# Kernel tuning notes

Hardware: AMD Instinct MI355X
Metric: run time of the kernel (lower is better)

The kernel has to match this reference:

```python
import jax, jax.numpy as jnp
import numpy as np

# Rain-rate balancing weights from the AccClearQPN repo; the loop uses the
# weight values themselves as the thresholds (faithful to compute_weights).
BALANCING_WEIGHTS = (1.0, 2.0, 5.0, 10.0, 30.0)
KSZ = 1  # kernel_size


def compute_weights(target, mask_f):
    w = jnp.full_like(target, BALANCING_WEIGHTS[0])
    for i in range(1, len(BALANCING_WEIGHTS)):
        w = w + (BALANCING_WEIGHTS[i] - BALANCING_WEIGHTS[i - 1]) * (
            target >= BALANCING_WEIGHTS[i]
        ).astype(target.dtype)
    return w * mask_f


def setup_inputs() -> dict:
    key = jax.random.key(0)
    k1, k2, k3 = jax.random.split(key, 3)
    S, B, H, W = 8, 16, 512, 512
    predicted = jax.random.uniform(k1, (S, B, H, W), dtype=jnp.float32) * 40.0
    target = jax.random.uniform(k2, (B, S, H, W), dtype=jnp.float32) * 40.0
    mask = jax.random.randint(k3, (B, S, H, W), 0, 2).astype(jnp.int32)
    return {"predicted": predicted, "target": target, "mask": mask}


def reference(predicted, target, mask):
    # predicted: [S,B,H,W]; target/mask: [B,S,H,W]
    S, B, H, W = predicted.shape
    pred = jnp.transpose(predicted, (1, 0, 2, 3))  # (B,S,H,W)
    weights = compute_weights(target, mask.astype(target.dtype))
    k = KSZ
    # zero-pad pred spatially; invalid shifted positions are masked to +inf below
    padded = jnp.pad(pred, ((0, 0), (0, 0), (k, k), (k, k)))
    ii = jnp.arange(H)
    jj = jnp.arange(W)
    # init = unshifted weighted abs diff (same as the (0,0) shift)
    loss2D = jnp.abs((target - pred) * weights)
    for x in range(-k, k + 1):
        vx = (ii + x >= 0) & (ii + x < H)
        for y in range(-k, k + 1):
            vy = (jj + y >= 0) & (jj + y < W)
            # pred sample at (i+x, j+y) for target pixel (i, j)
            pshift = padded[..., k + x : k + x + H, k + y : k + y + W]
            l = jnp.abs((target - pshift) * weights)
            l = jnp.where(vx[:, None] & vy[None, :], l, jnp.inf)
            loss2D = jnp.minimum(loss2D, l)
    return jnp.mean(loss2D)
```

## Files before the change

### kernel.cpp

```cpp
#include <hip/hip_runtime.h>

constexpr int S_DIM = 8;
constexpr int B_DIM = 16;
constexpr int H = 512;
constexpr int W = 512;
constexpr int PLANE = H * W;
constexpr long long NTOT = (long long)S_DIM * B_DIM * H * W;
constexpr int NGROUPS = (int)(NTOT / 4);
constexpr int GROUPS_PER_ROW = W / 4;
constexpr int GROUPS_PER_PLANE = PLANE / 4;

__device__ __forceinline__ float weight_of(float t) {
    float w = 1.0f;
    if (t >= 2.0f)  w = 2.0f;
    if (t >= 5.0f)  w = 5.0f;
    if (t >= 10.0f) w = 10.0f;
    if (t >= 30.0f) w = 30.0f;
    return w;
}

__device__ __forceinline__ float min3(float a, float b, float c) {
    return fminf(fminf(a, b), c);
}

__global__ __launch_bounds__(256)
void wmae_main(const float* __restrict__ pred,
               const float* __restrict__ targ,
               const int*   __restrict__ mask,
               double*      __restrict__ ws_sum) {
    const float BIG = 1e30f;
    float acc = 0.0f;

    const int stride = gridDim.x * blockDim.x;
    for (int gi = blockIdx.x * blockDim.x + threadIdx.x; gi < NGROUPS; gi += stride) {
        const int pl  = gi >> 16;
        const int rem = gi & (GROUPS_PER_PLANE - 1);
        const int row = rem >> 7;
        const int grp = rem & (GROUPS_PER_ROW - 1);
        const int j0  = grp << 2;

        const int b = pl >> 3;
        const int s = pl & 7;

        const size_t toff = (size_t)pl * PLANE + (size_t)row * W + j0;
        const float4 t4 = *reinterpret_cast<const float4*>(targ + toff);
        const int4   m4 = *reinterpret_cast<const int4*>(mask + toff);

        const float w0 = weight_of(t4.x) * (float)m4.x;
        const float w1 = weight_of(t4.y) * (float)m4.y;
        const float w2 = weight_of(t4.z) * (float)m4.z;
        const float w3 = weight_of(t4.w) * (float)m4.w;

        const float* pp = pred + (size_t)(s * B_DIM + b) * PLANE;

        float mn0 = BIG, mn1 = BIG, mn2 = BIG, mn3 = BIG;

        const int r_lo = (row > 0)     ? row - 1 : row;
        const int r_hi = (row < H - 1) ? row + 1 : row;

        for (int r = r_lo; r <= r_hi; ++r) {
            const float* pr = pp + (size_t)r * W + j0;
            const float4 p4 = *reinterpret_cast<const float4*>(pr);
            const float pv0 = (grp > 0)                  ? pr[-1] : BIG;
            const float pv5 = (grp < GROUPS_PER_ROW - 1) ? pr[4]  : BIG;
            const float pv1 = p4.x, pv2 = p4.y, pv3 = p4.z, pv4 = p4.w;

            mn0 = fminf(mn0, min3(fabsf(t4.x - pv0), fabsf(t4.x - pv1), fabsf(t4.x - pv2)));
            mn1 = fminf(mn1, min3(fabsf(t4.y - pv1), fabsf(t4.y - pv2), fabsf(t4.y - pv3)));
            mn2 = fminf(mn2, min3(fabsf(t4.z - pv2), fabsf(t4.z - pv3), fabsf(t4.z - pv4)));
            mn3 = fminf(mn3, min3(fabsf(t4.w - pv3), fabsf(t4.w - pv4), fabsf(t4.w - pv5)));
        }

        acc += w0 * mn0 + w1 * mn1 + w2 * mn2 + w3 * mn3;
    }

    #pragma unroll
    for (int off = 32; off > 0; off >>= 1)
        acc += __shfl_down(acc, off);

    __shared__ float wsum[4];
    const int wid  = threadIdx.x >> 6;
    const int lane = threadIdx.x & 63;
    if (lane == 0) wsum[wid] = acc;
    __syncthreads();
    if (threadIdx.x == 0) {
        const float bsum = wsum[0] + wsum[1] + wsum[2] + wsum[3];
        atomicAdd(ws_sum, (double)bsum);
    }
}

__global__ void wmae_finalize(const double* __restrict__ ws_sum,
                              float* __restrict__ out) {
    out[0] = (float)(ws_sum[0] / (double)NTOT);
}

extern "C" void kernel_launch(void* const* d_in, const int* in_sizes, int n_in,
                              void* d_out, int out_size, void* d_ws, size_t ws_size,
                              hipStream_t stream) {
    const float* predicted = (const float*)d_in[0];
    const float* target    = (const float*)d_in[1];
    const int*   mask      = (const int*)d_in[2];
    float* out  = (float*)d_out;
    double* wsd = (double*)d_ws;

    hipMemsetAsync(wsd, 0, sizeof(double), stream);
    wmae_main<<<2048, 256, 0, stream>>>(predicted, target, mask, wsd);
    wmae_finalize<<<1, 1, 0, stream>>>(wsd, out);
}
```

Measured before the change: 363.6 us.

## Assign wave per 4-row strip, reuse pred rows in registers, fuse finalize

Each wavefront now processes a 4-row strip of a plane, with each lane covering 8 columns. A rolling three-row register window keeps pred rows for reuse, and horizontal neighbours come from lane shuffles instead of extra unaligned loads. This cuts the redundant pred reads that the old per-group three-row loop made. The separate finalize kernel is replaced by a last-block-done counter inside the main kernel, which removes one launch but relies on correct fence and atomic ordering.

Measured after the change: 421.2 us. +15.8%, slower.

```diff
diff --git a/kernel.cpp b/kernel.cpp
--- a/kernel.cpp
+++ b/kernel.cpp
@@ -6,9 +6,14 @@
 constexpr int W = 512;
 constexpr int PLANE = H * W;
 constexpr long long NTOT = (long long)S_DIM * B_DIM * H * W;
-constexpr int NGROUPS = (int)(NTOT / 4);
-constexpr int GROUPS_PER_ROW = W / 4;
-constexpr int GROUPS_PER_PLANE = PLANE / 4;
+constexpr int ROWS = 4;
+constexpr int RBLKS = H / ROWS;
+constexpr int NPLANES = S_DIM * B_DIM;
+constexpr int NTASKS = NPLANES * RBLKS;
+constexpr int NBLOCKS = 2048;
+constexpr int NWAVES = NBLOCKS * 4;
+constexpr int TASKS_PER_WAVE = NTASKS / NWAVES;
+constexpr float BIG = 1e30f;
 
 __device__ __forceinline__ float weight_of(float t) {
     float w = 1.0f;
@@ -19,59 +24,109 @@
     return w;
 }
 
-__device__ __forceinline__ float min3(float a, float b, float c) {
+__device__ __forceinline__ float min3f(float a, float b, float c) {
     return fminf(fminf(a, b), c);
+}
+
+struct PRow {
+    float p[8];
+    float l, r;
+};
+
+__device__ __forceinline__ void load_prow(const float* __restrict__ q, int lane, PRow& w) {
+    const float4 a = *reinterpret_cast<const float4*>(q);
+    const float4 b = *reinterpret_cast<const float4*>(q + 4);
+    w.p[0] = a.x; w.p[1] = a.y; w.p[2] = a.z; w.p[3] = a.w;
+    w.p[4] = b.x; w.p[5] = b.y; w.p[6] = b.z; w.p[7] = b.w;
+    w.l = __shfl_up(b.w, 1);
+    w.r = __shfl_down(a.x, 1);
+    if (lane == 0)  w.l = BIG;
+    if (lane == 63) w.r = BIG;
+}
+
+__device__ __forceinline__ void accum_row(const PRow& pw, const float (&t)[8], float (&mn)[8]) {
+    mn[0] = fminf(mn[0], min3f(fabsf(t[0] - pw.l),
+                               fabsf(t[0] - pw.p[0]),
+                               fabsf(t[0] - pw.p[1])));
+    #pragma unroll
+    for (int c = 1; c < 7; ++c)
+        mn[c] = fminf(mn[c], min3f(fabsf(t[c] - pw.p[c - 1]),
+                                   fabsf(t[c] - pw.p[c]),
+                                   fabsf(t[c] - pw.p[c + 1])));
+    mn[7] = fminf(mn[7], min3f(fabsf(t[7] - pw.p[6]),
+                               fabsf(t[7] - pw.p[7]),
+                               fabsf(t[7] - pw.r)));
 }
 
 __global__ __launch_bounds__(256)
 void wmae_main(const float* __restrict__ pred,
                const float* __restrict__ targ,
                const int*   __restrict__ mask,
-               double*      __restrict__ ws_sum) {
-    const float BIG = 1e30f;
+               double*      __restrict__ ws_sum,
+               float*       __restrict__ out) {
+    const int tid  = threadIdx.x;
+    const int lane = tid & 63;
+    const int wv   = blockIdx.x * 4 + (tid >> 6);
+    const int col0 = lane * 8;
+
     float acc = 0.0f;
 
-    const int stride = gridDim.x * blockDim.x;
-    for (int gi = blockIdx.x * blockDim.x + threadIdx.x; gi < NGROUPS; gi += stride) {
-        const int pl  = gi >> 16;
-        const int rem = gi & (GROUPS_PER_PLANE - 1);
-        const int row = rem >> 7;
-        const int grp = rem & (GROUPS_PER_ROW - 1);
-        const int j0  = grp << 2;
+    #pragma unroll
+    for (int ti = 0; ti < TASKS_PER_WAVE; ++ti) {
+        const int tt = wv + ti * NWAVES;
+        const int pl = tt >> 7;
+        const int r0 = (tt & (RBLKS - 1)) * ROWS;
+        const int b  = pl >> 3;
+        const int s  = pl & 7;
 
-        const int b = pl >> 3;
-        const int s = pl & 7;
+        const float* __restrict__ P = pred + (size_t)(s * B_DIM + b) * PLANE + col0;
+        const float* __restrict__ T = targ + (size_t)pl * PLANE + col0;
+        const int*   __restrict__ M = mask + (size_t)pl * PLANE + col0;
 
-        const size_t toff = (size_t)pl * PLANE + (size_t)row * W + j0;
-        const float4 t4 = *reinterpret_cast<const float4*>(targ + toff);
-        const int4   m4 = *reinterpret_cast<const int4*>(mask + toff);
+        PRow w0, w1, w2;
+        load_prow(P + (size_t)(r0 > 0 ? r0 - 1 : 0) * W, lane, w0);
+        load_prow(P + (size_t)r0 * W, lane, w1);
 
-        const float w0 = weight_of(t4.x) * (float)m4.x;
-        const float w1 = weight_of(t4.y) * (float)m4.y;
-        const float w2 = weight_of(t4.z) * (float)m4.z;
-        const float w3 = weight_of(t4.w) * (float)m4.w;
+        #pragma unroll
+        for (int rr = 0; rr < ROWS; ++rr) {
+            const int r = r0 + rr;
+            PRow& wm = (rr % 3 == 0) ? w0 : (rr % 3 == 1) ? w1 : w2;
+            PRow& wc = (rr % 3 == 0) ? w1 : (rr % 3 == 1) ? w2 : w0;
+            PRow& wp = (rr % 3 == 0) ? w2 : (rr % 3 == 1) ? w0 : w1;
 
-        const float* pp = pred + (size_t)(s * B_DIM + b) * PLANE;
+            load_prow(P + (size_t)(r + 1 < H ? r + 1 : H - 1) * W, lane, wp);
 
-        float mn0 = BIG, mn1 = BIG, mn2 = BIG, mn3 = BIG;
+            const float* Tr = T + (size_t)r * W;
+            const int*   Mr = M + (size_t)r * W;
+            const float4 ta = *reinterpret_cast<const float4*>(Tr);
+            const float4 tb = *reinterpret_cast<const float4*>(Tr + 4);
+            const int4   ma = *reinterpret_cast<const int4*>(Mr);
+            const int4   mb = *reinterpret_cast<const int4*>(Mr + 4);
 
-        const int r_lo = (row > 0)     ? row - 1 : row;
-        const int r_hi = (row < H - 1) ? row + 1 : row;
+            const float t[8] = {ta.x, ta.y, ta.z, ta.w, tb.x, tb.y, tb.z, tb.w};
+            float wgt[8];
+            wgt[0] = weight_of(t[0]) * (float)ma.x;
+            wgt[1] = weight_of(t[1]) * (float)ma.y;
+            wgt[2] = weight_of(t[2]) * (float)ma.z;
+            wgt[3] = weight_of(t[3]) * (float)ma.w;
+            wgt[4] = weight_of(t[4]) * (float)mb.x;
+            wgt[5] = weight_of(t[5]) * (float)mb.y;
+            wgt[6] = weight_of(t[6]) * (float)mb.z;
+            wgt[7] = weight_of(t[7]) * (float)mb.w;
 
-        for (int r = r_lo; r <= r_hi; ++r) {
-            const float* pr = pp + (size_t)r * W + j0;
-            const float4 p4 = *reinterpret_cast<const float4*>(pr);
-            const float pv0 = (grp > 0)                  ? pr[-1] : BIG;
-            const float pv5 = (grp < GROUPS_PER_ROW - 1) ? pr[4]  : BIG;
-            const float pv1 = p4.x, pv2 = p4.y, pv3 = p4.z, pv4 = p4.w;
+            float mn[8];
+            #pragma unroll
+            for (int c = 0; c < 8; ++c) mn[c] = BIG;
 
-            mn0 = fminf(mn0, min3(fabsf(t4.x - pv0), fabsf(t4.x - pv1), fabsf(t4.x - pv2)));
-            mn1 = fminf(mn1, min3(fabsf(t4.y - pv1), fabsf(t4.y - pv2), fabsf(t4.y - pv3)));
-            mn2 = fminf(mn2, min3(fabsf(t4.z - pv2), fabsf(t4.z - pv3), fabsf(t4.z - pv4)));
-            mn3 = fminf(mn3, min3(fabsf(t4.w - pv3), fabsf(t4.w - pv4), fabsf(t4.w - pv5)));
+            if (rr > 0 || r0 > 0) accum_row(wm, t, mn);
+            accum_row(wc, t, mn);
+            if (r + 1 < H)        accum_row(wp, t, mn);
+
+            float rs = 0.0f;
+            #pragma unroll
+            for (int c = 0; c < 8; ++c) rs += wgt[c] * mn[c];
+            acc += rs;
         }
-
-        acc += w0 * mn0 + w1 * mn1 + w2 * mn2 + w3 * mn3;
     }
 
     #pragma unroll
@@ -79,19 +134,21 @@
         acc += __shfl_down(acc, off);
 
     __shared__ float wsum[4];
-    const int wid  = threadIdx.x >> 6;
-    const int lane = threadIdx.x & 63;
+    const int wid = tid >> 6;
     if (lane == 0) wsum[wid] = acc;
     __syncthreads();
-    if (threadIdx.x == 0) {
+
+    if (tid == 0) {
         const float bsum = wsum[0] + wsum[1] + wsum[2] + wsum[3];
         atomicAdd(ws_sum, (double)bsum);
+        __threadfence();
+        unsigned* ctr = reinterpret_cast<unsigned*>(ws_sum) + 2;
+        const unsigned prev = atomicAdd(ctr, 1u);
+        if (prev == (unsigned)gridDim.x - 1u) {
+            const double total = atomicAdd(ws_sum, 0.0);
+            out[0] = (float)(total / (double)NTOT);
+        }
     }
-}
-
-__global__ void wmae_finalize(const double* __restrict__ ws_sum,
-                              float* __restrict__ out) {
-    out[0] = (float)(ws_sum[0] / (double)NTOT);
 }
 
 extern "C" void kernel_launch(void* const* d_in, const int* in_sizes, int n_in,
@@ -100,10 +157,9 @@
     const float* predicted = (const float*)d_in[0];
     const float* target    = (const float*)d_in[1];
     const int*   mask      = (const int*)d_in[2];
-    float* out  = (float*)d_out;
+    float*  out = (float*)d_out;
     double* wsd = (double*)d_ws;
 
-    hipMemsetAsync(wsd, 0, sizeof(double), stream);
-    wmae_main<<<2048, 256, 0, stream>>>(predicted, target, mask, wsd);
-    wmae_finalize<<<1, 1, 0, stream>>>(wsd, out);
+    hipMemsetAsync(wsd, 0, 16, stream);
+    wmae_main<<<NBLOCKS, 256, 0, stream>>>(predicted, target, mask, wsd, out);
 }
```

## Process 16-pixel chunks per thread with all stencil loads issued upfront

Applied to the files above, without the earlier changes.

Each thread now handles a 16-wide chunk instead of 4, loading target, mask and three prediction rows as float4 vectors before computing. The aim is more memory-level parallelism and fewer redundant halo loads per output. The single atomic accumulator is also spread over 64 slots, which a 64-lane finalize kernel then reduces, to cut atomic contention. The wider chunks raise register pressure and make per-thread accesses strided by 64 bytes, which may hurt coalescing.

After: 364.2 us. About the same (+0.2%).

```diff
diff --git a/kernel.cpp b/kernel.cpp
--- a/kernel.cpp
+++ b/kernel.cpp
@@ -6,9 +6,15 @@
 constexpr int W = 512;
 constexpr int PLANE = H * W;
 constexpr long long NTOT = (long long)S_DIM * B_DIM * H * W;
-constexpr int NGROUPS = (int)(NTOT / 4);
-constexpr int GROUPS_PER_ROW = W / 4;
-constexpr int GROUPS_PER_PLANE = PLANE / 4;
+constexpr int NBLOCKS = 2048;
+constexpr int TPB = 256;
+constexpr int NTHREADS = NBLOCKS * TPB;
+constexpr int CHUNK = 16;
+constexpr int NCHUNK = (int)(NTOT / CHUNK);
+constexpr int CPR = W / CHUNK;
+constexpr int CPP = PLANE / CHUNK;
+constexpr float BIG = 1e30f;
+constexpr int NSLOT = 64;
 
 __device__ __forceinline__ float weight_of(float t) {
     float w = 1.0f;
@@ -19,79 +25,143 @@
     return w;
 }
 
-__device__ __forceinline__ float min3(float a, float b, float c) {
+__device__ __forceinline__ float min3f(float a, float b, float c) {
     return fminf(fminf(a, b), c);
 }
 
-__global__ __launch_bounds__(256)
+__global__ __launch_bounds__(TPB)
 void wmae_main(const float* __restrict__ pred,
                const float* __restrict__ targ,
                const int*   __restrict__ mask,
-               double*      __restrict__ ws_sum) {
-    const float BIG = 1e30f;
+               double*      __restrict__ slots) {
+    const int tid = threadIdx.x;
     float acc = 0.0f;
 
-    const int stride = gridDim.x * blockDim.x;
-    for (int gi = blockIdx.x * blockDim.x + threadIdx.x; gi < NGROUPS; gi += stride) {
-        const int pl  = gi >> 16;
-        const int rem = gi & (GROUPS_PER_PLANE - 1);
-        const int row = rem >> 7;
-        const int grp = rem & (GROUPS_PER_ROW - 1);
-        const int j0  = grp << 2;
+    #pragma unroll 1
+    for (int c = blockIdx.x * TPB + tid; c < NCHUNK; c += NTHREADS) {
+        const int pl  = c >> 14;
+        const int rem = c & (CPP - 1);
+        const int row = rem >> 5;
+        const int cx  = rem & (CPR - 1);
+        const int b   = pl >> 3;
+        const int s   = pl & 7;
 
-        const int b = pl >> 3;
-        const int s = pl & 7;
+        const size_t tb = (size_t)pl * PLANE + (size_t)row * W + cx * CHUNK;
+        const float* __restrict__ T  = targ + tb;
+        const int*   __restrict__ M  = mask + tb;
+        const float* __restrict__ Pc = pred + (size_t)(s * B_DIM + b) * PLANE
+                                            + (size_t)row * W + cx * CHUNK;
+        const float* __restrict__ Pm = Pc + ((row > 0)     ? -W : 0);
+        const float* __restrict__ Pp = Pc + ((row < H - 1) ?  W : 0);
+        const int lo = (cx > 0)       ? -1    : 0;
+        const int ro = (cx < CPR - 1) ? CHUNK : CHUNK - 1;
 
-        const size_t toff = (size_t)pl * PLANE + (size_t)row * W + j0;
-        const float4 t4 = *reinterpret_cast<const float4*>(targ + toff);
-        const int4   m4 = *reinterpret_cast<const int4*>(mask + toff);
+        const float4 t0 = *reinterpret_cast<const float4*>(T);
+        const float4 t1 = *reinterpret_cast<const float4*>(T + 4);
+        const float4 t2 = *reinterpret_cast<const float4*>(T + 8);
+        const float4 t3 = *reinterpret_cast<const float4*>(T + 12);
+        const int4   q0 = *reinterpret_cast<const int4*>(M);
+        const int4   q1 = *reinterpret_cast<const int4*>(M + 4);
+        const int4   q2 = *reinterpret_cast<const int4*>(M + 8);
+        const int4   q3 = *reinterpret_cast<const int4*>(M + 12);
+        const float4 pc0 = *reinterpret_cast<const float4*>(Pc);
+        const float4 pc1 = *reinterpret_cast<const float4*>(Pc + 4);
+        const float4 pc2 = *reinterpret_cast<const float4*>(Pc + 8);
+        const float4 pc3 = *reinterpret_cast<const float4*>(Pc + 12);
+        const float  pcl = Pc[lo], pcr = Pc[ro];
+        const float4 pa0 = *reinterpret_cast<const float4*>(Pm);
+        const float4 pa1 = *reinterpret_cast<const float4*>(Pm + 4);
+        const float4 pa2 = *reinterpret_cast<const float4*>(Pm + 8);
+        const float4 pa3 = *reinterpret_cast<const float4*>(Pm + 12);
+        const float  pal = Pm[lo], par = Pm[ro];
+        const float4 pb0 = *reinterpret_cast<const float4*>(Pp);
+        const float4 pb1 = *reinterpret_cast<const float4*>(Pp + 4);
+        const float4 pb2 = *reinterpret_cast<const float4*>(Pp + 8);
+        const float4 pb3 = *reinterpret_cast<const float4*>(Pp + 12);
+        const float  pbl = Pp[lo], pbr = Pp[ro];
 
-        const float w0 = weight_of(t4.x) * (float)m4.x;
-        const float w1 = weight_of(t4.y) * (float)m4.y;
-        const float w2 = weight_of(t4.z) * (float)m4.z;
-        const float w3 = weight_of(t4.w) * (float)m4.w;
+        const float tt[16] = {t0.x,t0.y,t0.z,t0.w, t1.x,t1.y,t1.z,t1.w,
+                              t2.x,t2.y,t2.z,t2.w, t3.x,t3.y,t3.z,t3.w};
+        const int   mm[16] = {q0.x,q0.y,q0.z,q0.w, q1.x,q1.y,q1.z,q1.w,
+                              q2.x,q2.y,q2.z,q2.w, q3.x,q3.y,q3.z,q3.w};
+        float ww[16];
+        #pragma unroll
+        for (int i = 0; i < 16; ++i) ww[i] = weight_of(tt[i]) * (float)mm[i];
 
-        const float* pp = pred + (size_t)(s * B_DIM + b) * PLANE;
+        const bool hasL = (cx > 0), hasR = (cx < CPR - 1);
 
-        float mn0 = BIG, mn1 = BIG, mn2 = BIG, mn3 = BIG;
+        float ctr[18];
+        ctr[0]  = hasL ? pcl : BIG;
+        ctr[17] = hasR ? pcr : BIG;
+        ctr[1]=pc0.x; ctr[2]=pc0.y; ctr[3]=pc0.z; ctr[4]=pc0.w;
+        ctr[5]=pc1.x; ctr[6]=pc1.y; ctr[7]=pc1.z; ctr[8]=pc1.w;
+        ctr[9]=pc2.x; ctr[10]=pc2.y; ctr[11]=pc2.z; ctr[12]=pc2.w;
+        ctr[13]=pc3.x; ctr[14]=pc3.y; ctr[15]=pc3.z; ctr[16]=pc3.w;
 
-        const int r_lo = (row > 0)     ? row - 1 : row;
-        const int r_hi = (row < H - 1) ? row + 1 : row;
+        float mn[16];
+        #pragma unroll
+        for (int i = 0; i < 16; ++i)
+            mn[i] = min3f(fabsf(tt[i] - ctr[i]),
+                          fabsf(tt[i] - ctr[i + 1]),
+                          fabsf(tt[i] - ctr[i + 2]));
 
-        for (int r = r_lo; r <= r_hi; ++r) {
-            const float* pr = pp + (size_t)r * W + j0;
-            const float4 p4 = *reinterpret_cast<const float4*>(pr);
-            const float pv0 = (grp > 0)                  ? pr[-1] : BIG;
-            const float pv5 = (grp < GROUPS_PER_ROW - 1) ? pr[4]  : BIG;
-            const float pv1 = p4.x, pv2 = p4.y, pv3 = p4.z, pv4 = p4.w;
-
-            mn0 = fminf(mn0, min3(fabsf(t4.x - pv0), fabsf(t4.x - pv1), fabsf(t4.x - pv2)));
-            mn1 = fminf(mn1, min3(fabsf(t4.y - pv1), fabsf(t4.y - pv2), fabsf(t4.y - pv3)));
-            mn2 = fminf(mn2, min3(fabsf(t4.z - pv2), fabsf(t4.z - pv3), fabsf(t4.z - pv4)));
-            mn3 = fminf(mn3, min3(fabsf(t4.w - pv3), fabsf(t4.w - pv4), fabsf(t4.w - pv5)));
+        if (row > 0) {
+            float up[18];
+            up[0]  = hasL ? pal : BIG;
+            up[17] = hasR ? par : BIG;
+            up[1]=pa0.x; up[2]=pa0.y; up[3]=pa0.z; up[4]=pa0.w;
+            up[5]=pa1.x; up[6]=pa1.y; up[7]=pa1.z; up[8]=pa1.w;
+            up[9]=pa2.x; up[10]=pa2.y; up[11]=pa2.z; up[12]=pa2.w;
+            up[13]=pa3.x; up[14]=pa3.y; up[15]=pa3.z; up[16]=pa3.w;
+            #pragma unroll
+            for (int i = 0; i < 16; ++i)
+                mn[i] = fminf(mn[i], min3f(fabsf(tt[i] - up[i]),
+                                           fabsf(tt[i] - up[i + 1]),
+                                           fabsf(tt[i] - up[i + 2])));
+        }
+        if (row < H - 1) {
+            float dn[18];
+            dn[0]  = hasL ? pbl : BIG;
+            dn[17] = hasR ? pbr : BIG;
+            dn[1]=pb0.x; dn[2]=pb0.y; dn[3]=pb0.z; dn[4]=pb0.w;
+            dn[5]=pb1.x; dn[6]=pb1.y; dn[7]=pb1.z; dn[8]=pb1.w;
+            dn[9]=pb2.x; dn[10]=pb2.y; dn[11]=pb2.z; dn[12]=pb2.w;
+            dn[13]=pb3.x; dn[14]=pb3.y; dn[15]=pb3.z; dn[16]=pb3.w;
+            #pragma unroll
+            for (int i = 0; i < 16; ++i)
+                mn[i] = fminf(mn[i], min3f(fabsf(tt[i] - dn[i]),
+                                           fabsf(tt[i] - dn[i + 1]),
+                                           fabsf(tt[i] - dn[i + 2])));
         }
 
-        acc += w0 * mn0 + w1 * mn1 + w2 * mn2 + w3 * mn3;
+        float rs = 0.0f;
+        #pragma unroll
+        for (int i = 0; i < 16; ++i) rs += ww[i] * mn[i];
+        acc += rs;
     }
 
     #pragma unroll
     for (int off = 32; off > 0; off >>= 1)
         acc += __shfl_down(acc, off);
 
-    __shared__ float wsum[4];
-    const int wid  = threadIdx.x >> 6;
-    const int lane = threadIdx.x & 63;
-    if (lane == 0) wsum[wid] = acc;
+    __shared__ float ws4[4];
+    const int wid  = tid >> 6;
+    const int lane = tid & 63;
+    if (lane == 0) ws4[wid] = acc;
     __syncthreads();
-    if (threadIdx.x == 0) {
-        const float bsum = wsum[0] + wsum[1] + wsum[2] + wsum[3];
-        atomicAdd(ws_sum, (double)bsum);
+    if (tid == 0) {
+        const float bsum = ws4[0] + ws4[1] + ws4[2] + ws4[3];
+        atomicAdd(&slots[blockIdx.x & (NSLOT - 1)], (double)bsum);
     }
 }
 
-__global__ void wmae_finalize(const double* __restrict__ ws_sum,
-                              float* __restrict__ out) {
-    out[0] = (float)(ws_sum[0] / (double)NTOT);
+__global__ void wmae_fin(const double* __restrict__ slots,
+                         float* __restrict__ out) {
+    double v = slots[threadIdx.x];
+    #pragma unroll
+    for (int off = 32; off > 0; off >>= 1)
+        v += __shfl_down(v, off);
+    if (threadIdx.x == 0) out[0] = (float)(v / (double)NTOT);
 }
 
 extern "C" void kernel_launch(void* const* d_in, const int* in_sizes, int n_in,
@@ -100,10 +170,10 @@
     const float* predicted = (const float*)d_in[0];
     const float* target    = (const float*)d_in[1];
     const int*   mask      = (const int*)d_in[2];
-    float* out  = (float*)d_out;
+    float*  out = (float*)d_out;
     double* wsd = (double*)d_ws;
 
-    hipMemsetAsync(wsd, 0, sizeof(double), stream);
-    wmae_main<<<2048, 256, 0, stream>>>(predicted, target, mask, wsd);
-    wmae_finalize<<<1, 1, 0, stream>>>(wsd, out);
+    hipMemsetAsync(wsd, 0, NSLOT * sizeof(double), stream);
+    wmae_main<<<NBLOCKS, TPB, 0, stream>>>(predicted, target, mask, wsd);
+    wmae_fin<<<1, 64, 0, stream>>>(wsd, out);
 }
```
